# Kernel optimization log

Measured on AMD Instinct MI355X. Metric: run time of the kernel, lower is better.

The kernel has to match this reference:

```python
import jax, jax.numpy as jnp
import numpy as np

SIG = [1, 1, 1, 1, -1]  # Cl(4,1)
NVEC = 5
GA = 1 << NVEC  # 32


def _build_gp_table():
    # Cayley table for the geometric product on blades indexed by bitmask.
    G = np.zeros((GA, GA, GA), np.float32)
    for a in range(GA):
        for b in range(GA):
            s = 0
            t = a >> 1
            while t:
                s += bin(t & b).count('1')
                t >>= 1
            sign = -1.0 if (s & 1) else 1.0
            common = a & b
            for i in range(NVEC):
                if (common >> i) & 1:
                    sign *= SIG[i]
            G[a, b, a ^ b] = sign
    return G

GP_TABLE = jnp.asarray(_build_gp_table())


def geometric_product(x, y):
    return jnp.einsum('...i,...j,ijk->...k', x, y, GP_TABLE)


def manifold_norm(x):
    # normalize each multivector onto the unit sphere in R^32
    return x / (jnp.linalg.norm(x, axis=-1, keepdims=True) + 1e-6)


def versor_linear(x, W, b):
    # channel mixing shared across multivector components: x [..., in, ga]
    return jnp.einsum('...ig,oi->...og', x, W) + b


def layer_norm2d(x, w, b):
    # LayerNorm over last two dims [D, ga] jointly
    mu = jnp.mean(x, axis=(-2, -1), keepdims=True)
    var = jnp.var(x, axis=(-2, -1), keepdims=True)
    return (x - mu) / jnp.sqrt(var + 1e-5) * w + b


def attention(x, Wq, bq, Wk, bk, Wv, bv, Wo, bo, n_heads):
    B, S, D, G = x.shape
    dh = D // n_heads
    q = versor_linear(x, Wq, bq).reshape(B, S, n_heads, dh, G)
    k = versor_linear(x, Wk, bk).reshape(B, S, n_heads, dh, G)
    v = versor_linear(x, Wv, bv).reshape(B, S, n_heads, dh, G)
    scale = 1.0 / np.sqrt(dh * G).astype(np.float32)
    scores = jnp.einsum('bshdg,bthdg->bhst', q, k) * scale
    probs = jax.nn.softmax(scores, axis=-1)
    o = jnp.einsum('bhst,bthdg->bshdg', probs, v).reshape(B, S, D, G)
    return versor_linear(o, Wo, bo)


N_HEADS = 8


def forward(x, Wq, bq, Wk, bk, Wv, bv, Wo, bo, ln1_w, ln1_b, ln2_w, ln2_b,
            gamma1, gamma2, W1, b1, W2, b2, Wr, br, Wc, bc):
    L = Wq.shape[0]
    for l in range(L):
        h = attention(layer_norm2d(x, ln1_w[l], ln1_b[l]),
                      Wq[l], bq[l], Wk[l], bk[l], Wv[l], bv[l], Wo[l], bo[l], N_HEADS)
        x = manifold_norm(x + gamma1[l] * h)
        m = versor_linear(layer_norm2d(x, ln2_w[l], ln2_b[l]), W1[l], b1[l])
        m = versor_linear(jnp.tanh(m), W2[l], b2[l])
        x = manifold_norm(x + gamma2[l] * m)
    # RecursiveRotorAccumulator: log(S)-step inclusive scan of rotors
    delta = versor_linear(x, Wr, br)
    rot = 0.5 * delta
    rot = rot.at[..., 0].add(1.0)
    rot = manifold_norm(rot)
    S = x.shape[1]
    step = 1
    while step < S:
        left = rot[:, :-step]
        right = rot[:, step:]
        comb = manifold_norm(geometric_product(right, left))
        rot = jnp.concatenate([rot[:, :step], comb], axis=1)
        step *= 2
    pooled = rot[:, -1]  # [B, D, ga]
    logits = pooled.reshape(pooled.shape[0], -1) @ Wc.T + bc
    return logits


def setup_inputs() -> dict:
    key = jax.random.key(0)
    B, S, D, G, L, NC = 8, 256, 64, GA, 4, 1000
    E = 4 * D  # expansion hidden
    ks = jax.random.split(key, 16)
    sd = 0.02
    inp = {
        'x': jax.random.normal(ks[0], (B, S, D, G), jnp.float32),
        'Wq': jax.random.normal(ks[1], (L, D, D), jnp.float32) * sd,
        'bq': jnp.zeros((L, D, G), jnp.float32),
        'Wk': jax.random.normal(ks[2], (L, D, D), jnp.float32) * sd,
        'bk': jnp.zeros((L, D, G), jnp.float32),
        'Wv': jax.random.normal(ks[3], (L, D, D), jnp.float32) * sd,
        'bv': jnp.zeros((L, D, G), jnp.float32),
        'Wo': jax.random.normal(ks[4], (L, D, D), jnp.float32) * sd,
        'bo': jnp.zeros((L, D, G), jnp.float32),
        'ln1_w': jnp.ones((L, D, G), jnp.float32),
        'ln1_b': jnp.zeros((L, D, G), jnp.float32),
        'ln2_w': jnp.ones((L, D, G), jnp.float32),
        'ln2_b': jnp.zeros((L, D, G), jnp.float32),
        'gamma1': 1e-5 * jnp.ones((L, D, G), jnp.float32),
        'gamma2': 1e-5 * jnp.ones((L, D, G), jnp.float32),
        'W1': jax.random.normal(ks[5], (L, E, D), jnp.float32) * sd,
        'b1': jnp.zeros((L, E, G), jnp.float32),
        'W2': jax.random.normal(ks[6], (L, D, E), jnp.float32) * sd,
        'b2': jnp.zeros((L, D, G), jnp.float32),
        'Wr': jax.random.normal(ks[7], (D, D), jnp.float32) * sd,
        'br': jnp.zeros((D, G), jnp.float32),
        'Wc': jax.random.normal(ks[8], (NC, D * G), jnp.float32) * sd,
        'bc': jnp.zeros((NC,), jnp.float32),
    }
    return inp


def reference(x, Wq, bq, Wk, bk, Wv, bv, Wo, bo, ln1_w, ln1_b, ln2_w, ln2_b,
              gamma1, gamma2, W1, b1, W2, b2, Wr, br, Wc, bc):
    return forward(x, Wq, bq, Wk, bk, Wv, bv, Wo, bo, ln1_w, ln1_b, ln2_w, ln2_b,
                   gamma1, gamma2, W1, b1, W2, b2, Wr, br, Wc, bc)
```

## Files before the change

### kernel.cpp

```cpp
#include <hip/hip_runtime.h>
#include <hip/hip_bf16.h>

constexpr int kB  = 8;
constexpr int kS  = 256;
constexpr int kD  = 64;
constexpr int kG  = 32;
constexpr int kE  = 256;
constexpr int kNH = 8;
constexpr int kHD = 256;
constexpr int kDG = kD * kG;
constexpr int kT  = kB * kS;
constexpr int kNC = 1000;

using bf16x8 = __attribute__((ext_vector_type(8))) short;
using f32x4  = __attribute__((ext_vector_type(4))) float;

__device__ __forceinline__ short f2bf(float f) {
    unsigned u = __float_as_uint(f);
    unsigned r = (u + 0x7FFFu + ((u >> 16) & 1u)) >> 16;
    return (short)r;
}

__device__ __forceinline__ float tanh_fast(float x) {
    float a = fabsf(x);
    float e = __expf(-2.f * a);
    float d = 1.f + e;
    float r = __builtin_amdgcn_rcpf(d);
    r = r * (2.f - d * r);
    float t = (1.f - e) * r;
    return copysignf(t, x);
}

__global__ __launch_bounds__(256) void cvtw_kernel(
    const float* __restrict__ Wq, const float* __restrict__ Wk,
    const float* __restrict__ Wv, const float* __restrict__ Wo,
    const float* __restrict__ W1, const float* __restrict__ W2,
    unsigned short* __restrict__ dst) {
    int idx = (blockIdx.x * 256 + threadIdx.x) * 4;
    const float* src; int off;
    if      (idx <  16384) { src = Wq; off = 0; }
    else if (idx <  32768) { src = Wk; off = 16384; }
    else if (idx <  49152) { src = Wv; off = 32768; }
    else if (idx <  65536) { src = Wo; off = 49152; }
    else if (idx < 131072) { src = W1; off = 65536; }
    else                   { src = W2; off = 131072; }
    const float4 v = *(const float4*)(src + (idx - off));
    *(short4*)&dst[idx] = make_short4(f2bf(v.x), f2bf(v.y), f2bf(v.z), f2bf(v.w));
}

__global__ __launch_bounds__(256) void ln_kernel(const float* __restrict__ Xin,
                                                 const float* __restrict__ w,
                                                 const float* __restrict__ b,
                                                 unsigned short* __restrict__ A) {
    int t = blockIdx.x, tid = threadIdx.x;
    const float* xp = Xin + (size_t)t * kDG;
    __shared__ float r1[256], r2[256];
    __shared__ short st[32 * 72];
    float v[8], s = 0.f, ss = 0.f;
#pragma unroll
    for (int j = 0; j < 8; j++) {
        float x = xp[tid + j * 256];
        v[j] = x; s += x; ss += x * x;
    }
    r1[tid] = s; r2[tid] = ss; __syncthreads();
    for (int o = 128; o > 0; o >>= 1) {
        if (tid < o) { r1[tid] += r1[tid + o]; r2[tid] += r2[tid + o]; }
        __syncthreads();
    }
    float mean = r1[0] * (1.f / kDG);
    float var  = r2[0] * (1.f / kDG) - mean * mean;
    float rstd = rsqrtf(var + 1e-5f);
#pragma unroll
    for (int j = 0; j < 8; j++) {
        int jj = tid + j * 256;
        float val = (v[j] - mean) * rstd * w[jj] + b[jj];
        st[(jj & 31) * 72 + (jj >> 5)] = f2bf(val);
    }
    __syncthreads();
    bf16x8 ov = *(const bf16x8*)&st[(tid >> 3) * 72 + (tid & 7) * 8];
    *(bf16x8*)&A[(size_t)t * kDG + tid * 8] = ov;
}

__device__ __forceinline__ void epi_res_mn_ln(
    const f32x4 (&acc)[4][2], const float* __restrict__ bias,
    const float* __restrict__ Xin, float* __restrict__ Xout,
    const float* __restrict__ gamma,
    const float* __restrict__ lnw, const float* __restrict__ lnb,
    unsigned short* __restrict__ Aout, int tok, int l16, int quad, bool do_ln) {
    const size_t tb = (size_t)tok * kDG;
    float xv[4][2][4];
    float s = 0.f, ss = 0.f;
#pragma unroll
    for (int mt = 0; mt < 4; ++mt)
#pragma unroll
        for (int r = 0; r < 4; ++r) {
            int o = mt * 16 + quad * 4 + r;
            float vv[2]; float sq = 0.f;
#pragma unroll
            for (int nt = 0; nt < 2; ++nt) {
                int g = nt * 16 + l16;
                float h = acc[mt][nt][r] + bias[o * kG + g];
                float v = Xin[tb + o * kG + g] + gamma[o * kG + g] * h;
                vv[nt] = v; sq = fmaf(v, v, sq);
            }
#pragma unroll
            for (int off = 1; off < 16; off <<= 1) sq += __shfl_xor(sq, off, 64);
            float rn = 1.f / (sqrtf(sq) + 1e-6f);
#pragma unroll
            for (int nt = 0; nt < 2; ++nt) {
                int g = nt * 16 + l16;
                float x = vv[nt] * rn;
                xv[mt][nt][r] = x;
                Xout[tb + o * kG + g] = x;
                s += x; ss = fmaf(x, x, ss);
            }
        }
    if (!do_ln) return;
#pragma unroll
    for (int off = 1; off < 64; off <<= 1) {
        s += __shfl_xor(s, off, 64); ss += __shfl_xor(ss, off, 64);
    }
    float mean = s * (1.f / kDG);
    float var  = ss * (1.f / kDG) - mean * mean;
    float rstd = rsqrtf(var + 1e-5f);
    unsigned short* aop = Aout + tb;
#pragma unroll
    for (int mt = 0; mt < 4; ++mt)
#pragma unroll
        for (int nt = 0; nt < 2; ++nt) {
            int g = nt * 16 + l16;
            int o0 = mt * 16 + quad * 4;
            short4 s4;
#pragma unroll
            for (int r = 0; r < 4; ++r) {
                int o = o0 + r;
                float lv = (xv[mt][nt][r] - mean) * rstd * lnw[o * kG + g] + lnb[o * kG + g];
                (&s4.x)[r] = f2bf(lv);
            }
            *(short4*)&aop[g * kD + o0] = s4;
        }
}

__global__ __launch_bounds__(256) void vlinT_kernel(const float* __restrict__ X,
                                                    const float* __restrict__ W,
                                                    const float* __restrict__ bias,
                                                    float* __restrict__ OutT) {
    __shared__ float sx[kDG];
    __shared__ float sw[kD * kD];
    int t = blockIdx.x, tid = threadIdx.x;
    const float* xp = X + (size_t)t * kDG;
    for (int j = tid; j < kDG; j += 256) sx[j] = xp[j];
    for (int j = tid; j < kD * kD; j += 256) sw[j] = W[j];
    __syncthreads();
    int g = tid & 31, ob = tid >> 5;
    int b = t >> 8, s = t & 255;
    float* op = OutT + ((size_t)b * kD * kS + s) * kG;
    for (int o = ob; o < kD; o += 8) {
        float acc = bias[o * kG + g];
        const float* wr = sw + o * kD;
#pragma unroll
        for (int i = 0; i < kD; i++) acc += wr[i] * sx[i * kG + g];
        op[(size_t)o * kS * kG + g] = acc;
    }
}

template<bool DO_LN>
__global__ __launch_bounds__(64) void mlp_fused_kernel(
    const unsigned short* __restrict__ A,
    const unsigned short* __restrict__ W1h,
    const float* __restrict__ b1,
    const unsigned short* __restrict__ W2h,
    const float* __restrict__ b2,
    float* __restrict__ X, const float* __restrict__ gamma,
    const float* __restrict__ lnw, const float* __restrict__ lnb,
    unsigned short* __restrict__ Aout) {
    __shared__ short sM[32 * 256];
    const int lane = threadIdx.x;
    const int l16 = lane & 15, quad = lane >> 4;
    const int tok = blockIdx.x;

    const unsigned short* xp = A + (size_t)tok * kDG;
    bf16x8 bfr[2][2];
#pragma unroll
    for (int c = 0; c < 2; ++c)
#pragma unroll
        for (int nt = 0; nt < 2; ++nt)
            bfr[c][nt] = *(const bf16x8*)&xp[(nt * 16 + l16) * kD + c * 32 + quad * 8];

    char* mwB = (char*)sM;

#pragma unroll
    for (int half = 0; half < 2; ++half) {
        f32x4 acc[8][2];
#pragma unroll
        for (int mt = 0; mt < 8; ++mt)
#pragma unroll
            for (int nt = 0; nt < 2; ++nt) acc[mt][nt] = (f32x4){0.f, 0.f, 0.f, 0.f};

#pragma unroll
        for (int mt = 0; mt < 8; ++mt)
#pragma unroll
            for (int c = 0; c < 2; ++c) {
                int e16 = half * 8 + mt;
                bf16x8 afr = *(const bf16x8*)&W1h[(e16 * 16 + l16) * kD + c * 32 + quad * 8];
#pragma unroll
                for (int nt = 0; nt < 2; ++nt)
                    acc[mt][nt] = __builtin_amdgcn_mfma_f32_16x16x32_bf16(afr, bfr[c][nt], acc[mt][nt], 0, 0, 0);
            }

#pragma unroll
        for (int mt = 0; mt < 8; ++mt)
#pragma unroll
            for (int nt = 0; nt < 2; ++nt) {
                int g = nt * 16 + l16;
                int e0 = (half * 8 + mt) * 16 + quad * 4;
                short4 s4;
#pragma unroll
                for (int r = 0; r < 4; ++r)
                    (&s4.x)[r] = f2bf(tanh_fast(acc[mt][nt][r] + b1[(e0 + r) * kG + g]));
                unsigned boff = (unsigned)g * 512u + (((unsigned)(e0 * 2)) ^ (((unsigned)g & 7u) << 4));
                *(short4*)(mwB + boff) = s4;
            }
    }

    f32x4 acc2[4][2];
#pragma unroll
    for (int mt = 0; mt < 4; ++mt)
#pragma unroll
        for (int nt = 0; nt < 2; ++nt) acc2[mt][nt] = (f32x4){0.f, 0.f, 0.f, 0.f};

#pragma unroll
    for (int c = 0; c < 8; ++c) {
        bf16x8 bq[2];
#pragma unroll
        for (int nt = 0; nt < 2; ++nt) {
            int g = nt * 16 + l16;
            unsigned boff = (unsigned)g * 512u + (((unsigned)(c * 64 + quad * 16)) ^ (((unsigned)g & 7u) << 4));
            bq[nt] = *(const bf16x8*)(mwB + boff);
        }
#pragma unroll
        for (int mt = 0; mt < 4; ++mt) {
            bf16x8 afr = *(const bf16x8*)&W2h[(mt * 16 + l16) * kE + c * 32 + quad * 8];
#pragma unroll
            for (int nt = 0; nt < 2; ++nt)
                acc2[mt][nt] = __builtin_amdgcn_mfma_f32_16x16x32_bf16(afr, bq[nt], acc2[mt][nt], 0, 0, 0);
        }
    }

    epi_res_mn_ln(acc2, b2, X, X, gamma, lnw, lnb, Aout, tok, l16, quad, DO_LN);
}

__global__ __launch_bounds__(256, 3) void gemmWo_fused_kernel(
    const unsigned short* __restrict__ X, const unsigned short* __restrict__ Wh,
    const float* __restrict__ bias,
    const float* __restrict__ Xin, const float* __restrict__ gamma,
    const float* __restrict__ lnw, const float* __restrict__ lnb,
    float* __restrict__ Xout, unsigned short* __restrict__ Aout) {
    constexpr int WS = 64 + 8;
    __shared__ short sW[64 * WS];

    const int tid = threadIdx.x, wave = tid >> 6, lane = tid & 63;
    const int l16 = lane & 15, quad = lane >> 4;
    const int tok = blockIdx.x * 4 + wave;

    for (int j = tid * 8; j < 64 * 64; j += 2048) {
        int o = j >> 6, i = j & 63;
        *(bf16x8*)&sW[o * WS + i] = *(const bf16x8*)(Wh + j);
    }

    const unsigned short* xp = X + (size_t)tok * kDG;
    bf16x8 bfr[2][2];
#pragma unroll
    for (int c = 0; c < 2; ++c)
#pragma unroll
        for (int nt = 0; nt < 2; ++nt)
            bfr[c][nt] = *(const bf16x8*)&xp[(nt * 16 + l16) * kD + c * 32 + quad * 8];
    __syncthreads();

    f32x4 acc[4][2];
#pragma unroll
    for (int mt = 0; mt < 4; ++mt)
#pragma unroll
        for (int nt = 0; nt < 2; ++nt) acc[mt][nt] = (f32x4){0.f, 0.f, 0.f, 0.f};

#pragma unroll
    for (int mt = 0; mt < 4; ++mt)
#pragma unroll
        for (int c = 0; c < 2; ++c) {
            bf16x8 afr = *(const bf16x8*)&sW[(mt * 16 + l16) * WS + c * 32 + quad * 8];
#pragma unroll
            for (int nt = 0; nt < 2; ++nt)
                acc[mt][nt] = __builtin_amdgcn_mfma_f32_16x16x32_bf16(afr, bfr[c][nt], acc[mt][nt], 0, 0, 0);
        }

    epi_res_mn_ln(acc, bias, Xin, Xout, gamma, lnw, lnb, Aout, tok, l16, quad, true);
}

__global__ __launch_bounds__(256, 3) void gemm_qkv_kernel(
    const unsigned short* __restrict__ X,
    const unsigned short* __restrict__ Wqh, const unsigned short* __restrict__ Wkh,
    const unsigned short* __restrict__ Wvh,
    const float* __restrict__ bq, const float* __restrict__ bk, const float* __restrict__ bv,
    unsigned short* __restrict__ Q, unsigned short* __restrict__ K, unsigned short* __restrict__ V) {
    constexpr int WS = 64 + 8;
    __shared__ short sW[3 * 64 * WS];

    const int tid = threadIdx.x, wave = tid >> 6, lane = tid & 63;
    const int l16 = lane & 15, quad = lane >> 4;
    const int tok = blockIdx.x * 4 + wave;

    const unsigned short* Wp[3] = {Wqh, Wkh, Wvh};
#pragma unroll
    for (int w = 0; w < 3; ++w)
        for (int j = tid * 8; j < 64 * 64; j += 2048) {
            int o = j >> 6, i = j & 63;
            *(bf16x8*)&sW[w * 64 * WS + o * WS + i] = *(const bf16x8*)(Wp[w] + j);
        }

    const unsigned short* xp = X + (size_t)tok * kDG;
    bf16x8 bfr[2][2];
#pragma unroll
    for (int c = 0; c < 2; ++c)
#pragma unroll
        for (int nt = 0; nt < 2; ++nt)
            bfr[c][nt] = *(const bf16x8*)&xp[(nt * 16 + l16) * kD + c * 32 + quad * 8];
    __syncthreads();

    f32x4 acc[3][4][2];
#pragma unroll
    for (int w = 0; w < 3; ++w)
#pragma unroll
        for (int mt = 0; mt < 4; ++mt)
#pragma unroll
            for (int nt = 0; nt < 2; ++nt) acc[w][mt][nt] = (f32x4){0.f, 0.f, 0.f, 0.f};

#pragma unroll
    for (int w = 0; w < 3; ++w)
#pragma unroll
        for (int mt = 0; mt < 4; ++mt)
#pragma unroll
            for (int c = 0; c < 2; ++c) {
                bf16x8 afr = *(const bf16x8*)&sW[w * 64 * WS + (mt * 16 + l16) * WS + c * 32 + quad * 8];
#pragma unroll
                for (int nt = 0; nt < 2; ++nt)
                    acc[w][mt][nt] = __builtin_amdgcn_mfma_f32_16x16x32_bf16(afr, bfr[c][nt], acc[w][mt][nt], 0, 0, 0);
            }

    unsigned short* Op[3] = {Q, K, V};
    const float* Bp[3] = {bq, bk, bv};
#pragma unroll
    for (int w = 0; w < 3; ++w) {
        unsigned short* op = Op[w] + (size_t)tok * kDG;
#pragma unroll
        for (int mt = 0; mt < 4; ++mt)
#pragma unroll
            for (int nt = 0; nt < 2; ++nt) {
                int g = nt * 16 + l16;
#pragma unroll
                for (int r = 0; r < 4; ++r) {
                    int o = mt * 16 + quad * 4 + r;
                    op[o * kG + g] = (unsigned short)f2bf(acc[w][mt][nt][r] + Bp[w][o * kG + g]);
                }
            }
    }
}

constexpr int QSTR = 264;
constexpr int VSTR = 40;

__global__ __launch_bounds__(256) void attn_mfma_kernel(const unsigned short* __restrict__ Q,
                                                        const unsigned short* __restrict__ K,
                                                        const unsigned short* __restrict__ V,
                                                        unsigned short* __restrict__ O) {
    __shared__ short sQ[64 * QSTR];
    __shared__ short sKV[2][256 * VSTR];

    const int qt = blockIdx.x, h = blockIdx.y, b = blockIdx.z;
    const int tid = threadIdx.x;
    const int wave = tid >> 6, lane = tid & 63;
    const int l16 = lane & 15, quad = lane >> 4;

    const size_t bh = (size_t)b * kS * kDG + (size_t)h * kHD;

#pragma unroll
    for (int it = 0; it < 8; ++it) {
        int j = it * 2048 + tid * 8;
        int row = j >> 8, col = j & 255;
        *(bf16x8*)&sQ[row * QSTR + col] =
            *(const bf16x8*)(Q + bh + (size_t)(qt * 64 + row) * kDG + col);
    }
#pragma unroll
    for (int it = 0; it < 4; ++it) {
        int j = it * 2048 + tid * 8;
        int row = j >> 8, col = j & 255;
        *(bf16x8*)&sKV[0][row * QSTR + col] =
            *(const bf16x8*)(K + bh + (size_t)row * kDG + col);
    }
    __syncthreads();

    bf16x8 afrag[8];
    {
        int row = wave * 16 + l16;
#pragma unroll
        for (int c = 0; c < 8; ++c)
            afrag[c] = *(const bf16x8*)&sQ[row * QSTR + c * 32 + quad * 8];
    }

    f32x4 acc[16];
#pragma unroll
    for (int i = 0; i < 16; ++i) acc[i] = (f32x4){0.f, 0.f, 0.f, 0.f};

    for (int kt = 0; kt < 8; ++kt) {
        bf16x8 kpre[4];
        if (kt < 7) {
#pragma unroll
            for (int it = 0; it < 4; ++it) {
                int j = it * 2048 + tid * 8;
                int row = j >> 8, col = j & 255;
                kpre[it] = *(const bf16x8*)(K + bh + (size_t)((kt + 1) * 32 + row) * kDG + col);
            }
        }
        const short* kb = sKV[kt & 1];
#pragma unroll
        for (int nt = 0; nt < 2; ++nt) {
            int key = nt * 16 + l16;
            f32x4 a = acc[kt * 2 + nt];
#pragma unroll
            for (int c = 0; c < 8; ++c) {
                bf16x8 bfrag = *(const bf16x8*)&kb[key * QSTR + c * 32 + quad * 8];
                a = __builtin_amdgcn_mfma_f32_16x16x32_bf16(afrag[c], bfrag, a, 0, 0, 0);
            }
            acc[kt * 2 + nt] = a;
        }
        if (kt < 7) {
            short* nb = sKV[(kt + 1) & 1];
#pragma unroll
            for (int it = 0; it < 4; ++it) {
                int j = it * 2048 + tid * 8;
                int row = j >> 8, col = j & 255;
                *(bf16x8*)&nb[row * QSTR + col] = kpre[it];
            }
            __syncthreads();
        }
    }

    float inv[4];
#pragma unroll
    for (int r = 0; r < 4; ++r) {
        float m = -1e30f;
#pragma unroll
        for (int t = 0; t < 16; ++t) m = fmaxf(m, acc[t][r]);
#pragma unroll
        for (int off = 1; off < 16; off <<= 1) m = fmaxf(m, __shfl_xor(m, off, 16));
        float s = 0.f;
#pragma unroll
        for (int t = 0; t < 16; ++t) {
            float p = __expf((acc[t][r] - m) * 0.0625f);
            acc[t][r] = p; s += p;
        }
#pragma unroll
        for (int off = 1; off < 16; off <<= 1) s += __shfl_xor(s, off, 16);
        inv[r] = 1.f / s;
    }

#pragma unroll
    for (int t = 0; t < 16; ++t)
#pragma unroll
        for (int r = 0; r < 4; ++r)
            sQ[(wave * 16 + quad * 4 + r) * QSTR + t * 16 + l16] = f2bf(acc[t][r]);

    {
        int kb = tid >> 5;
#pragma unroll
        for (int it = 0; it < 2; ++it) {
            int db = (tid & 31) + it * 32;
            short4 vr[4];
#pragma unroll
            for (int r = 0; r < 4; ++r)
                vr[r] = *(const short4*)(V + bh + (size_t)(kb * 4 + r) * kDG + db * 4);
#pragma unroll
            for (int i = 0; i < 4; ++i) {
                short4 p = make_short4((&vr[0].x)[i], (&vr[1].x)[i],
                                       (&vr[2].x)[i], (&vr[3].x)[i]);
                *(short4*)&sKV[0][(db * 4 + i) * VSTR + kb * 4] = p;
            }
        }
    }
    __syncthreads();

    f32x4 oacc[16];
#pragma unroll
    for (int i = 0; i < 16; ++i) oacc[i] = (f32x4){0.f, 0.f, 0.f, 0.f};

    for (int vt = 0; vt < 8; ++vt) {
        short4 vpre[8];
        if (vt < 7) {
            int kb = tid >> 5;
#pragma unroll
            for (int it = 0; it < 2; ++it) {
                int db = (tid & 31) + it * 32;
#pragma unroll
                for (int r = 0; r < 4; ++r)
                    vpre[it * 4 + r] = *(const short4*)(V + bh + (size_t)((vt + 1) * 32 + kb * 4 + r) * kDG + db * 4);
            }
        }
        const short* vb = sKV[vt & 1];
        bf16x8 pfrag = *(const bf16x8*)&sQ[(wave * 16 + l16) * QSTR + vt * 32 + quad * 8];
#pragma unroll
        for (int dt = 0; dt < 16; ++dt) {
            bf16x8 vfrag = *(const bf16x8*)&vb[(dt * 16 + l16) * VSTR + quad * 8];
            oacc[dt] = __builtin_amdgcn_mfma_f32_16x16x32_bf16(pfrag, vfrag, oacc[dt], 0, 0, 0);
        }
        if (vt < 7) {
            short* nb = sKV[(vt + 1) & 1];
            int kb = tid >> 5;
#pragma unroll
            for (int it = 0; it < 2; ++it) {
                int db = (tid & 31) + it * 32;
#pragma unroll
                for (int i = 0; i < 4; ++i) {
                    short4 p = make_short4((&vpre[it * 4 + 0].x)[i], (&vpre[it * 4 + 1].x)[i],
                                           (&vpre[it * 4 + 2].x)[i], (&vpre[it * 4 + 3].x)[i]);
                    *(short4*)&nb[(db * 4 + i) * VSTR + kb * 4] = p;
                }
            }
            __syncthreads();
        }
    }

    {
        const size_t ob = (size_t)(b * kS + qt * 64 + wave * 16 + quad * 4) * kDG + h * 8;
#pragma unroll
        for (int gg = 0; gg < 2; ++gg) {
            int g = gg * 16 + l16;
#pragma unroll
            for (int r = 0; r < 4; ++r) {
                bf16x8 pk;
#pragma unroll
                for (int k = 0; k < 8; ++k)
                    pk[k] = f2bf(oacc[k * 2 + gg][r] * inv[r]);
                *(bf16x8*)&O[ob + (size_t)r * kDG + g * kD] = pk;
            }
        }
    }
}

constexpr int pc_ce(unsigned v) { int c = 0; while (v) { c += v & 1; v >>= 1; } return c; }
constexpr unsigned gp_mask_ce(int a) {
    unsigned m = 0;
    for (int c = 0; c < 32; ++c) {
        int b = a ^ c;
        int s = (a & b) >> 4;
        for (int t = a >> 1; t; t >>= 1) s += pc_ce(t & b);
        if (s & 1) m |= (1u << c);
    }
    return m;
}

template<int A>
__device__ __forceinline__ void gp_term(const float* x, const float* y, float* acc) {
    constexpr unsigned m = gp_mask_ce(A);
    const float xa = x[A], nxa = -xa;
#pragma unroll
    for (int c = 0; c < 32; ++c)
        acc[c] = fmaf(((m >> c) & 1u) ? nxa : xa, y[A ^ c], acc[c]);
}

__device__ __forceinline__ void gp_mn_t(const float* x, const float* y, float* out) {
    float acc[32];
#pragma unroll
    for (int c = 0; c < 32; ++c) acc[c] = 0.f;
    gp_term<0>(x, y, acc);  gp_term<1>(x, y, acc);  gp_term<2>(x, y, acc);  gp_term<3>(x, y, acc);
    gp_term<4>(x, y, acc);  gp_term<5>(x, y, acc);  gp_term<6>(x, y, acc);  gp_term<7>(x, y, acc);
    gp_term<8>(x, y, acc);  gp_term<9>(x, y, acc);  gp_term<10>(x, y, acc); gp_term<11>(x, y, acc);
    gp_term<12>(x, y, acc); gp_term<13>(x, y, acc); gp_term<14>(x, y, acc); gp_term<15>(x, y, acc);
    gp_term<16>(x, y, acc); gp_term<17>(x, y, acc); gp_term<18>(x, y, acc); gp_term<19>(x, y, acc);
    gp_term<20>(x, y, acc); gp_term<21>(x, y, acc); gp_term<22>(x, y, acc); gp_term<23>(x, y, acc);
    gp_term<24>(x, y, acc); gp_term<25>(x, y, acc); gp_term<26>(x, y, acc); gp_term<27>(x, y, acc);
    gp_term<28>(x, y, acc); gp_term<29>(x, y, acc); gp_term<30>(x, y, acc); gp_term<31>(x, y, acc);
    float ss = 0.f;
#pragma unroll
    for (int c = 0; c < 32; ++c) ss = fmaf(acc[c], acc[c], ss);
    float r = 1.f / (sqrtf(ss) + 1e-6f);
#pragma unroll
    for (int c = 0; c < 32; ++c) out[c] = acc[c] * r;
}

__device__ __forceinline__ void leaf_load(const float* base, float* v) {
#pragma unroll
    for (int i = 0; i < 8; ++i) {
        const float4 f = *(const float4*)(base + i * 4);
        v[i * 4 + 0] = 0.5f * f.x; v[i * 4 + 1] = 0.5f * f.y;
        v[i * 4 + 2] = 0.5f * f.z; v[i * 4 + 3] = 0.5f * f.w;
    }
    v[0] += 1.f;
    float ss = 0.f;
#pragma unroll
    for (int c = 0; c < 32; ++c) ss = fmaf(v[c], v[c], ss);
    float r = 1.f / (sqrtf(ss) + 1e-6f);
#pragma unroll
    for (int c = 0; c < 32; ++c) v[c] *= r;
}

__global__ __launch_bounds__(256) void scanreg_kernel(const float* __restrict__ DT,
                                                      float* __restrict__ pooled) {
    const int wave = threadIdx.x >> 6, lane = threadIdx.x & 63;
    const int seq = blockIdx.x * 4 + wave;
    const float* base = DT + ((size_t)seq * kS + lane * 4) * kG;

    float R[32], Y[32], P[32], Xa[32], Yb[32];

    leaf_load(base, R);
    for (int j = 1; j < 4; ++j) {
        leaf_load(base + j * kG, Y);
        gp_mn_t(Y, R, R);
    }

    for (int step = 1; step < 64; step <<= 1) {
        const bool up = lane & step;
#pragma unroll
        for (int c = 0; c < 32; ++c) P[c] = __shfl_xor(R[c], step, 64);
#pragma unroll
        for (int c = 0; c < 32; ++c) {
            Xa[c] = up ? R[c] : P[c];
            Yb[c] = up ? P[c] : R[c];
        }
        gp_mn_t(Xa, Yb, R);
    }

    if (lane == 0) {
        float* op = pooled + (size_t)seq * kG;
#pragma unroll
        for (int i = 0; i < 8; ++i)
            *(float4*)(op + i * 4) = make_float4(R[i * 4], R[i * 4 + 1], R[i * 4 + 2], R[i * 4 + 3]);
    }
}

__global__ __launch_bounds__(256) void cls2_kernel(const float* __restrict__ P,
                                                   const float* __restrict__ Wc,
                                                   const float* __restrict__ bc,
                                                   float* __restrict__ out) {
    __shared__ float sp[kB * kDG];
    const int tid = threadIdx.x, wave = tid >> 6, lane = tid & 63;
    for (int j = tid * 4; j < kB * kDG; j += 1024)
        *(float4*)&sp[j] = *(const float4*)(P + j);
    __syncthreads();

    const int c = blockIdx.x * 4 + wave;
    const float* w = Wc + (size_t)c * kDG;
    float acc[kB];
#pragma unroll
    for (int b = 0; b < kB; ++b) acc[b] = 0.f;
#pragma unroll
    for (int cc = 0; cc < 8; ++cc) {
        const float4 w4 = *(const float4*)(w + cc * 256 + lane * 4);
#pragma unroll
        for (int b = 0; b < kB; ++b) {
            const float4 p4 = *(const float4*)&sp[b * kDG + cc * 256 + lane * 4];
            acc[b] += w4.x * p4.x + w4.y * p4.y + w4.z * p4.z + w4.w * p4.w;
        }
    }
#pragma unroll
    for (int b = 0; b < kB; ++b)
#pragma unroll
        for (int off = 32; off > 0; off >>= 1) acc[b] += __shfl_xor(acc[b], off, 64);
    if (lane == 0) {
        float bias = bc[c];
#pragma unroll
        for (int b = 0; b < kB; ++b) out[b * kNC + c] = acc[b] + bias;
    }
}

extern "C" void kernel_launch(void* const* d_in, const int* in_sizes, int n_in,
                              void* d_out, int out_size, void* d_ws, size_t ws_size,
                              hipStream_t stream) {
    const float* x_in = (const float*)d_in[0];
    const float* Wq   = (const float*)d_in[1];
    const float* bq   = (const float*)d_in[2];
    const float* Wk   = (const float*)d_in[3];
    const float* bk   = (const float*)d_in[4];
    const float* Wv   = (const float*)d_in[5];
    const float* bv   = (const float*)d_in[6];
    const float* Wo   = (const float*)d_in[7];
    const float* bo   = (const float*)d_in[8];
    const float* ln1w = (const float*)d_in[9];
    const float* ln1b = (const float*)d_in[10];
    const float* ln2w = (const float*)d_in[11];
    const float* ln2b = (const float*)d_in[12];
    const float* gm1  = (const float*)d_in[13];
    const float* gm2  = (const float*)d_in[14];
    const float* W1   = (const float*)d_in[15];
    const float* b1   = (const float*)d_in[16];
    const float* W2   = (const float*)d_in[17];
    const float* b2   = (const float*)d_in[18];
    const float* Wr   = (const float*)d_in[19];
    const float* br   = (const float*)d_in[20];
    const float* Wc   = (const float*)d_in[21];
    const float* bc   = (const float*)d_in[22];

    const size_t NEL = (size_t)kT * kDG;
    float* F  = (float*)d_ws;
    float* X  = F;
    unsigned short* Abf = (unsigned short*)(F + NEL);
    unsigned short* Qh = (unsigned short*)(F + 2 * NEL);
    unsigned short* Kh = (unsigned short*)(F + 3 * NEL);
    unsigned short* Vh = (unsigned short*)(F + 4 * NEL);
    unsigned short* Wb = (unsigned short*)(F + 5 * NEL);
    float* pooled = F + 2 * NEL;
    float* DT = F + NEL;

    cvtw_kernel<<<192, 256, 0, stream>>>(Wq, Wk, Wv, Wo, W1, W2, Wb);
    unsigned short* Wqh = Wb;
    unsigned short* Wkh = Wb + 16384;
    unsigned short* Wvh = Wb + 32768;
    unsigned short* Woh = Wb + 49152;
    unsigned short* W1h = Wb + 65536;
    unsigned short* W2h = Wb + 131072;

    ln_kernel<<<kT, 256, 0, stream>>>(x_in, ln1w, ln1b, Abf);

    for (int l = 0; l < 4; l++) {
        gemm_qkv_kernel<<<kT / 4, 256, 0, stream>>>(Abf,
            Wqh + l * 4096, Wkh + l * 4096, Wvh + l * 4096,
            bq + l * kDG, bk + l * kDG, bv + l * kDG, Qh, Kh, Vh);
        attn_mfma_kernel<<<dim3(4, kNH, kB), 256, 0, stream>>>(Qh, Kh, Vh, Abf);
        gemmWo_fused_kernel<<<kT / 4, 256, 0, stream>>>(Abf, Woh + l * 4096, bo + l * kDG,
            l == 0 ? x_in : X, gm1 + l * kDG, ln2w + l * kDG, ln2b + l * kDG, X, Abf);
        if (l < 3)
            mlp_fused_kernel<true><<<kT, 64, 0, stream>>>(Abf,
                W1h + l * 16384, b1 + l * kE * kG, W2h + l * 16384, b2 + l * kDG,
                X, gm2 + l * kDG, ln1w + (l + 1) * kDG, ln1b + (l + 1) * kDG, Abf);
        else
            mlp_fused_kernel<false><<<kT, 64, 0, stream>>>(Abf,
                W1h + l * 16384, b1 + l * kE * kG, W2h + l * 16384, b2 + l * kDG,
                X, gm2 + l * kDG, nullptr, nullptr, nullptr);
    }

    vlinT_kernel<<<kT, 256, 0, stream>>>(X, Wr, br, DT);
    scanreg_kernel<<<kB * kD / 4, 256, 0, stream>>>(DT, pooled);
    cls2_kernel<<<kNC / 4, 256, 0, stream>>>(pooled, Wc, bc, (float*)d_out);
}
```

Baseline: 555.8 us.

## Store residual stream transposed and split MLP across two waves

```diff
diff --git a/kernel.cpp b/kernel.cpp
--- a/kernel.cpp
+++ b/kernel.cpp
@@ -48,19 +48,47 @@
     *(short4*)&dst[idx] = make_short4(f2bf(v.x), f2bf(v.y), f2bf(v.z), f2bf(v.w));
 }
 
+__global__ __launch_bounds__(256) void prep_tr_kernel(
+    const float* __restrict__ bq, const float* __restrict__ bk,
+    const float* __restrict__ bv, const float* __restrict__ bo,
+    const float* __restrict__ b2, const float* __restrict__ gm1,
+    const float* __restrict__ gm2, const float* __restrict__ ln2w,
+    const float* __restrict__ ln2b, const float* __restrict__ ln1w,
+    const float* __restrict__ ln1b, const float* __restrict__ b1,
+    float* __restrict__ dst) {
+    __shared__ float lt[32 * 257];
+    const int a = blockIdx.x >> 2, l = blockIdx.x & 3;
+    const float* srcs[12] = {bq, bk, bv, bo, b2, gm1, gm2, ln2w, ln2b, ln1w, ln1b, b1};
+    const int R  = (a == 11) ? 256 : 64;
+    const int sh = (a == 11) ? 8 : 6;
+    const float* src = srcs[a] + (size_t)l * R * 32;
+    float* out = dst + a * 8192 + l * R * 32;
+    const int tid = threadIdx.x;
+    for (int j = tid; j < R * 32; j += 256) lt[(j & 31) * (R + 1) + (j >> 5)] = src[j];
+    __syncthreads();
+    for (int k = tid; k < R * 32; k += 256) {
+        int g = k >> sh, r = k & (R - 1);
+        out[k] = lt[g * (R + 1) + r];
+    }
+}
+
 __global__ __launch_bounds__(256) void ln_kernel(const float* __restrict__ Xin,
                                                  const float* __restrict__ w,
                                                  const float* __restrict__ b,
-                                                 unsigned short* __restrict__ A) {
+                                                 unsigned short* __restrict__ A,
+                                                 float* __restrict__ XT) {
     int t = blockIdx.x, tid = threadIdx.x;
     const float* xp = Xin + (size_t)t * kDG;
     __shared__ float r1[256], r2[256];
     __shared__ short st[32 * 72];
+    __shared__ float xf[32 * 68];
     float v[8], s = 0.f, ss = 0.f;
 #pragma unroll
     for (int j = 0; j < 8; j++) {
         float x = xp[tid + j * 256];
         v[j] = x; s += x; ss += x * x;
+        int jj = tid + j * 256;
+        xf[(jj & 31) * 68 + (jj >> 5)] = x;
     }
     r1[tid] = s; r2[tid] = ss; __syncthreads();
     for (int o = 128; o > 0; o >>= 1) {
@@ -79,77 +107,86 @@
     __syncthreads();
     bf16x8 ov = *(const bf16x8*)&st[(tid >> 3) * 72 + (tid & 7) * 8];
     *(bf16x8*)&A[(size_t)t * kDG + tid * 8] = ov;
-}
-
-__device__ __forceinline__ void epi_res_mn_ln(
-    const f32x4 (&acc)[4][2], const float* __restrict__ bias,
-    const float* __restrict__ Xin, float* __restrict__ Xout,
-    const float* __restrict__ gamma,
-    const float* __restrict__ lnw, const float* __restrict__ lnb,
-    unsigned short* __restrict__ Aout, int tok, int l16, int quad, bool do_ln) {
-    const size_t tb = (size_t)tok * kDG;
-    float xv[4][2][4];
-    float s = 0.f, ss = 0.f;
-#pragma unroll
-    for (int mt = 0; mt < 4; ++mt)
-#pragma unroll
-        for (int r = 0; r < 4; ++r) {
-            int o = mt * 16 + quad * 4 + r;
-            float vv[2]; float sq = 0.f;
-#pragma unroll
-            for (int nt = 0; nt < 2; ++nt) {
-                int g = nt * 16 + l16;
-                float h = acc[mt][nt][r] + bias[o * kG + g];
-                float v = Xin[tb + o * kG + g] + gamma[o * kG + g] * h;
-                vv[nt] = v; sq = fmaf(v, v, sq);
-            }
-#pragma unroll
-            for (int off = 1; off < 16; off <<= 1) sq += __shfl_xor(sq, off, 64);
-            float rn = 1.f / (sqrtf(sq) + 1e-6f);
-#pragma unroll
-            for (int nt = 0; nt < 2; ++nt) {
-                int g = nt * 16 + l16;
-                float x = vv[nt] * rn;
-                xv[mt][nt][r] = x;
-                Xout[tb + o * kG + g] = x;
-                s += x; ss = fmaf(x, x, ss);
-            }
-        }
-    if (!do_ln) return;
-#pragma unroll
-    for (int off = 1; off < 64; off <<= 1) {
-        s += __shfl_xor(s, off, 64); ss += __shfl_xor(ss, off, 64);
-    }
-    float mean = s * (1.f / kDG);
-    float var  = ss * (1.f / kDG) - mean * mean;
-    float rstd = rsqrtf(var + 1e-5f);
-    unsigned short* aop = Aout + tb;
-#pragma unroll
-    for (int mt = 0; mt < 4; ++mt)
+    const int row = tid >> 3, col = (tid & 7) * 8;
+    float* xo = XT + (size_t)t * kDG + tid * 8;
+    *(float4*)(xo + 0) = *(const float4*)&xf[row * 68 + col + 0];
+    *(float4*)(xo + 4) = *(const float4*)&xf[row * 68 + col + 4];
+}
+
+template<int MT>
+__device__ __forceinline__ void epiT(
+    const f32x4 (&acc)[MT][2], const float* __restrict__ bT,
+    float* __restrict__ XTp, const float* __restrict__ gT,
+    int l16, int quad, int obase,
+    float& s, float& ss, float (&xv)[MT][2][4]) {
+    s = 0.f; ss = 0.f;
+#pragma unroll
+    for (int mt = 0; mt < MT; ++mt) {
+        int o0 = obase + mt * 16 + quad * 4;
+        float vv[2][4];
 #pragma unroll
         for (int nt = 0; nt < 2; ++nt) {
             int g = nt * 16 + l16;
-            int o0 = mt * 16 + quad * 4;
+            const float4 b4 = *(const float4*)&bT[g * kD + o0];
+            const float4 g4 = *(const float4*)&gT[g * kD + o0];
+            const float4 xi = *(const float4*)&XTp[g * kD + o0];
+#pragma unroll
+            for (int r = 0; r < 4; ++r)
+                vv[nt][r] = (&xi.x)[r] + (&g4.x)[r] * (acc[mt][nt][r] + (&b4.x)[r]);
+        }
+        float rn[4];
+#pragma unroll
+        for (int r = 0; r < 4; ++r) {
+            float sq = vv[0][r] * vv[0][r] + vv[1][r] * vv[1][r];
+#pragma unroll
+            for (int off = 1; off < 16; off <<= 1) sq += __shfl_xor(sq, off, 64);
+            rn[r] = 1.f / (sqrtf(sq) + 1e-6f);
+        }
+#pragma unroll
+        for (int nt = 0; nt < 2; ++nt) {
+            int g = nt * 16 + l16;
+            float4 xo;
+#pragma unroll
+            for (int r = 0; r < 4; ++r) {
+                float x = vv[nt][r] * rn[r];
+                (&xo.x)[r] = x; xv[mt][nt][r] = x;
+                s += x; ss = fmaf(x, x, ss);
+            }
+            *(float4*)&XTp[g * kD + o0] = xo;
+        }
+    }
+}
+
+template<int MT>
+__device__ __forceinline__ void lnT(
+    const float (&xv)[MT][2][4], const float* __restrict__ lwT,
+    const float* __restrict__ lbT, unsigned short* __restrict__ Aoutp,
+    int l16, int quad, int obase, float mean, float rstd) {
+#pragma unroll
+    for (int mt = 0; mt < MT; ++mt)
+#pragma unroll
+        for (int nt = 0; nt < 2; ++nt) {
+            int g = nt * 16 + l16;
+            int o0 = obase + mt * 16 + quad * 4;
+            const float4 w4 = *(const float4*)&lwT[g * kD + o0];
+            const float4 b4 = *(const float4*)&lbT[g * kD + o0];
             short4 s4;
 #pragma unroll
-            for (int r = 0; r < 4; ++r) {
-                int o = o0 + r;
-                float lv = (xv[mt][nt][r] - mean) * rstd * lnw[o * kG + g] + lnb[o * kG + g];
-                (&s4.x)[r] = f2bf(lv);
-            }
-            *(short4*)&aop[g * kD + o0] = s4;
-        }
-}
-
-__global__ __launch_bounds__(256) void vlinT_kernel(const float* __restrict__ X,
+            for (int r = 0; r < 4; ++r)
+                (&s4.x)[r] = f2bf((xv[mt][nt][r] - mean) * rstd * (&w4.x)[r] + (&b4.x)[r]);
+            *(short4*)&Aoutp[g * kD + o0] = s4;
+        }
+}
+
+__global__ __launch_bounds__(256) void vlinT_kernel(const float* __restrict__ XT,
                                                     const float* __restrict__ W,
                                                     const float* __restrict__ bias,
                                                     float* __restrict__ OutT) {
-    __shared__ float sx[kDG];
+    __shared__ float sx[32 * 65];
     __shared__ float sw[kD * kD];
     int t = blockIdx.x, tid = threadIdx.x;
-    const float* xp = X + (size_t)t * kDG;
-    for (int j = tid; j < kDG; j += 256) sx[j] = xp[j];
+    const float* xp = XT + (size_t)t * kDG;
+    for (int j = tid; j < kDG; j += 256) sx[(j >> 6) * 65 + (j & 63)] = xp[j];
     for (int j = tid; j < kD * kD; j += 256) sw[j] = W[j];
     __syncthreads();
     int g = tid & 31, ob = tid >> 5;
@@ -159,23 +196,26 @@
         float acc = bias[o * kG + g];
         const float* wr = sw + o * kD;
 #pragma unroll
-        for (int i = 0; i < kD; i++) acc += wr[i] * sx[i * kG + g];
+        for (int i = 0; i < kD; i++) acc += wr[i] * sx[g * 65 + i];
         op[(size_t)o * kS * kG + g] = acc;
     }
 }
 
 template<bool DO_LN>
-__global__ __launch_bounds__(64) void mlp_fused_kernel(
+__global__ __launch_bounds__(128, 4) void mlp_fused_kernel(
     const unsigned short* __restrict__ A,
     const unsigned short* __restrict__ W1h,
-    const float* __restrict__ b1,
+    const float* __restrict__ b1T,
     const unsigned short* __restrict__ W2h,
-    const float* __restrict__ b2,
-    float* __restrict__ X, const float* __restrict__ gamma,
-    const float* __restrict__ lnw, const float* __restrict__ lnb,
+    const float* __restrict__ b2T,
+    float* __restrict__ XT, const float* __restrict__ gmT,
+    const float* __restrict__ lwT, const float* __restrict__ lbT,
     unsigned short* __restrict__ Aout) {
-    __shared__ short sM[32 * 256];
-    const int lane = threadIdx.x;
+    constexpr int MS = 264;
+    __shared__ short sM[32 * MS];
+    __shared__ float sred[4];
+    const int tid = threadIdx.x;
+    const int w = tid >> 6, lane = tid & 63;
     const int l16 = lane & 15, quad = lane >> 4;
     const int tok = blockIdx.x;
 
@@ -187,45 +227,40 @@
         for (int nt = 0; nt < 2; ++nt)
             bfr[c][nt] = *(const bf16x8*)&xp[(nt * 16 + l16) * kD + c * 32 + quad * 8];
 
-    char* mwB = (char*)sM;
-
-#pragma unroll
-    for (int half = 0; half < 2; ++half) {
-        f32x4 acc[8][2];
-#pragma unroll
-        for (int mt = 0; mt < 8; ++mt)
-#pragma unroll
-            for (int nt = 0; nt < 2; ++nt) acc[mt][nt] = (f32x4){0.f, 0.f, 0.f, 0.f};
-
-#pragma unroll
-        for (int mt = 0; mt < 8; ++mt)
-#pragma unroll
-            for (int c = 0; c < 2; ++c) {
-                int e16 = half * 8 + mt;
-                bf16x8 afr = *(const bf16x8*)&W1h[(e16 * 16 + l16) * kD + c * 32 + quad * 8];
-#pragma unroll
-                for (int nt = 0; nt < 2; ++nt)
-                    acc[mt][nt] = __builtin_amdgcn_mfma_f32_16x16x32_bf16(afr, bfr[c][nt], acc[mt][nt], 0, 0, 0);
-            }
-
-#pragma unroll
-        for (int mt = 0; mt < 8; ++mt)
-#pragma unroll
-            for (int nt = 0; nt < 2; ++nt) {
-                int g = nt * 16 + l16;
-                int e0 = (half * 8 + mt) * 16 + quad * 4;
-                short4 s4;
-#pragma unroll
-                for (int r = 0; r < 4; ++r)
-                    (&s4.x)[r] = f2bf(tanh_fast(acc[mt][nt][r] + b1[(e0 + r) * kG + g]));
-                unsigned boff = (unsigned)g * 512u + (((unsigned)(e0 * 2)) ^ (((unsigned)g & 7u) << 4));
-                *(short4*)(mwB + boff) = s4;
-            }
-    }
-
-    f32x4 acc2[4][2];
-#pragma unroll
-    for (int mt = 0; mt < 4; ++mt)
+    f32x4 acc[8][2];
+#pragma unroll
+    for (int mt = 0; mt < 8; ++mt)
+#pragma unroll
+        for (int nt = 0; nt < 2; ++nt) acc[mt][nt] = (f32x4){0.f, 0.f, 0.f, 0.f};
+
+#pragma unroll
+    for (int mt = 0; mt < 8; ++mt)
+#pragma unroll
+        for (int c = 0; c < 2; ++c) {
+            bf16x8 afr = *(const bf16x8*)&W1h[((w * 8 + mt) * 16 + l16) * kD + c * 32 + quad * 8];
+#pragma unroll
+            for (int nt = 0; nt < 2; ++nt)
+                acc[mt][nt] = __builtin_amdgcn_mfma_f32_16x16x32_bf16(afr, bfr[c][nt], acc[mt][nt], 0, 0, 0);
+        }
+
+#pragma unroll
+    for (int mt = 0; mt < 8; ++mt)
+#pragma unroll
+        for (int nt = 0; nt < 2; ++nt) {
+            int g = nt * 16 + l16;
+            int e0 = (w * 8 + mt) * 16 + quad * 4;
+            const float4 b4 = *(const float4*)&b1T[g * kE + e0];
+            short4 s4;
+#pragma unroll
+            for (int r = 0; r < 4; ++r)
+                (&s4.x)[r] = f2bf(tanh_fast(acc[mt][nt][r] + (&b4.x)[r]));
+            *(short4*)&sM[g * MS + e0] = s4;
+        }
+    __syncthreads();
+
+    f32x4 acc2[2][2];
+#pragma unroll
+    for (int mt = 0; mt < 2; ++mt)
 #pragma unroll
         for (int nt = 0; nt < 2; ++nt) acc2[mt][nt] = (f32x4){0.f, 0.f, 0.f, 0.f};
 
@@ -233,29 +268,41 @@
     for (int c = 0; c < 8; ++c) {
         bf16x8 bq[2];
 #pragma unroll
-        for (int nt = 0; nt < 2; ++nt) {
-            int g = nt * 16 + l16;
-            unsigned boff = (unsigned)g * 512u + (((unsigned)(c * 64 + quad * 16)) ^ (((unsigned)g & 7u) << 4));
-            bq[nt] = *(const bf16x8*)(mwB + boff);
-        }
-#pragma unroll
-        for (int mt = 0; mt < 4; ++mt) {
-            bf16x8 afr = *(const bf16x8*)&W2h[(mt * 16 + l16) * kE + c * 32 + quad * 8];
+        for (int nt = 0; nt < 2; ++nt)
+            bq[nt] = *(const bf16x8*)&sM[(nt * 16 + l16) * MS + c * 32 + quad * 8];
+#pragma unroll
+        for (int mt = 0; mt < 2; ++mt) {
+            bf16x8 afr = *(const bf16x8*)&W2h[(w * 32 + mt * 16 + l16) * kE + c * 32 + quad * 8];
 #pragma unroll
             for (int nt = 0; nt < 2; ++nt)
                 acc2[mt][nt] = __builtin_amdgcn_mfma_f32_16x16x32_bf16(afr, bq[nt], acc2[mt][nt], 0, 0, 0);
         }
     }
 
-    epi_res_mn_ln(acc2, b2, X, X, gamma, lnw, lnb, Aout, tok, l16, quad, DO_LN);
+    const size_t tb = (size_t)tok * kDG;
+    float xv[2][2][4]; float s, ss;
+    epiT<2>(acc2, b2T, XT + tb, gmT, l16, quad, w * 32, s, ss, xv);
+    if (DO_LN) {
+#pragma unroll
+        for (int off = 1; off < 64; off <<= 1) {
+            s += __shfl_xor(s, off, 64); ss += __shfl_xor(ss, off, 64);
+        }
+        if (lane == 0) { sred[w] = s; sred[2 + w] = ss; }
+        __syncthreads();
+        float st = sred[0] + sred[1], sst = sred[2] + sred[3];
+        float mean = st * (1.f / kDG);
+        float var  = sst * (1.f / kDG) - mean * mean;
+        float rstd = rsqrtf(var + 1e-5f);
+        lnT<2>(xv, lwT, lbT, Aout + tb, l16, quad, w * 32, mean, rstd);
+    }
 }
 
 __global__ __launch_bounds__(256, 3) void gemmWo_fused_kernel(
     const unsigned short* __restrict__ X, const unsigned short* __restrict__ Wh,
-    const float* __restrict__ bias,
-    const float* __restrict__ Xin, const float* __restrict__ gamma,
-    const float* __restrict__ lnw, const float* __restrict__ lnb,
-    float* __restrict__ Xout, unsigned short* __restrict__ Aout) {
+    const float* __restrict__ bT,
+    float* __restrict__ XT, const float* __restrict__ gmT,
+    const float* __restrict__ lwT, const float* __restrict__ lbT,
+    unsigned short* __restrict__ Aout) {
     constexpr int WS = 64 + 8;
     __shared__ short sW[64 * WS];
 
@@ -293,14 +340,24 @@
                 acc[mt][nt] = __builtin_amdgcn_mfma_f32_16x16x32_bf16(afr, bfr[c][nt], acc[mt][nt], 0, 0, 0);
         }
 
-    epi_res_mn_ln(acc, bias, Xin, Xout, gamma, lnw, lnb, Aout, tok, l16, quad, true);
+    const size_t tb = (size_t)tok * kDG;
+    float xv[4][2][4]; float s, ss;
+    epiT<4>(acc, bT, XT + tb, gmT, l16, quad, 0, s, ss, xv);
+#pragma unroll
+    for (int off = 1; off < 64; off <<= 1) {
+        s += __shfl_xor(s, off, 64); ss += __shfl_xor(ss, off, 64);
+    }
+    float mean = s * (1.f / kDG);
+    float var  = ss * (1.f / kDG) - mean * mean;
+    float rstd = rsqrtf(var + 1e-5f);
+    lnT<4>(xv, lwT, lbT, Aout + tb, l16, quad, 0, mean, rstd);
 }
 
 __global__ __launch_bounds__(256, 3) void gemm_qkv_kernel(
     const unsigned short* __restrict__ X,
     const unsigned short* __restrict__ Wqh, const unsigned short* __restrict__ Wkh,
     const unsigned short* __restrict__ Wvh,
-    const float* __restrict__ bq, const float* __restrict__ bk, const float* __restrict__ bv,
+    const float* __restrict__ bqT, const float* __restrict__ bkT, const float* __restrict__ bvT,
     unsigned short* __restrict__ Q, unsigned short* __restrict__ K, unsigned short* __restrict__ V) {
     constexpr int WS = 64 + 8;
     __shared__ short sW[3 * 64 * WS];
@@ -347,7 +404,7 @@
             }
 
     unsigned short* Op[3] = {Q, K, V};
-    const float* Bp[3] = {bq, bk, bv};
+    const float* Bp[3] = {bqT, bkT, bvT};
 #pragma unroll
     for (int w = 0; w < 3; ++w) {
         unsigned short* op = Op[w] + (size_t)tok * kDG;
@@ -356,11 +413,11 @@
 #pragma unroll
             for (int nt = 0; nt < 2; ++nt) {
                 int g = nt * 16 + l16;
-#pragma unroll
-                for (int r = 0; r < 4; ++r) {
-                    int o = mt * 16 + quad * 4 + r;
-                    op[o * kG + g] = (unsigned short)f2bf(acc[w][mt][nt][r] + Bp[w][o * kG + g]);
-                }
+                int o0 = mt * 16 + quad * 4;
+                const float4 b4 = *(const float4*)&Bp[w][g * kD + o0];
+#pragma unroll
+                for (int r = 0; r < 4; ++r)
+                    op[(o0 + r) * kG + g] = (unsigned short)f2bf(acc[w][mt][nt][r] + (&b4.x)[r]);
             }
     }
 }
@@ -700,16 +757,19 @@
 
     const size_t NEL = (size_t)kT * kDG;
     float* F  = (float*)d_ws;
-    float* X  = F;
+    float* XT = F;
     unsigned short* Abf = (unsigned short*)(F + NEL);
     unsigned short* Qh = (unsigned short*)(F + 2 * NEL);
     unsigned short* Kh = (unsigned short*)(F + 3 * NEL);
     unsigned short* Vh = (unsigned short*)(F + 4 * NEL);
     unsigned short* Wb = (unsigned short*)(F + 5 * NEL);
+    float* PT = F + 3 * NEL + NEL / 2;
     float* pooled = F + 2 * NEL;
     float* DT = F + NEL;
 
     cvtw_kernel<<<192, 256, 0, stream>>>(Wq, Wk, Wv, Wo, W1, W2, Wb);
+    prep_tr_kernel<<<48, 256, 0, stream>>>(bq, bk, bv, bo, b2, gm1, gm2,
+                                           ln2w, ln2b, ln1w, ln1b, b1, PT);
     unsigned short* Wqh = Wb;
     unsigned short* Wkh = Wb + 16384;
     unsigned short* Wvh = Wb + 32768;
@@ -717,26 +777,39 @@
     unsigned short* W1h = Wb + 65536;
     unsigned short* W2h = Wb + 131072;
 
-    ln_kernel<<<kT, 256, 0, stream>>>(x_in, ln1w, ln1b, Abf);
+    auto bqT   = [&](int l) { return PT + 0     + l * 2048; };
+    auto bkT   = [&](int l) { return PT + 8192  + l * 2048; };
+    auto bvT   = [&](int l) { return PT + 16384 + l * 2048; };
+    auto boT   = [&](int l) { return PT + 24576 + l * 2048; };
+    auto b2T   = [&](int l) { return PT + 32768 + l * 2048; };
+    auto gm1T  = [&](int l) { return PT + 40960 + l * 2048; };
+    auto gm2T  = [&](int l) { return PT + 49152 + l * 2048; };
+    auto ln2wT = [&](int l) { return PT + 57344 + l * 2048; };
+    auto ln2bT = [&](int l) { return PT + 65536 + l * 2048; };
+    auto ln1wT = [&](int l) { return PT + 73728 + l * 2048; };
+    auto ln1bT = [&](int l) { return PT + 81920 + l * 2048; };
+    auto b1T   = [&](int l) { return PT + 90112 + l * 8192; };
+
+    ln_kernel<<<kT, 256, 0, stream>>>(x_in, ln1w, ln1b, Abf, XT);
 
     for (int l = 0; l < 4; l++) {
         gemm_qkv_kernel<<<kT / 4, 256, 0, stream>>>(Abf,
             Wqh + l * 4096, Wkh + l * 4096, Wvh + l * 4096,
-            bq + l * kDG, bk + l * kDG, bv + l * kDG, Qh, Kh, Vh);
+            bqT(l), bkT(l), bvT(l), Qh, Kh, Vh);
         attn_mfma_kernel<<<dim3(4, kNH, kB), 256, 0, stream>>>(Qh, Kh, Vh, Abf);
-        gemmWo_fused_kernel<<<kT / 4, 256, 0, stream>>>(Abf, Woh + l * 4096, bo + l * kDG,
-            l == 0 ? x_in : X, gm1 + l * kDG, ln2w + l * kDG, ln2b + l * kDG, X, Abf);
+        gemmWo_fused_kernel<<<kT / 4, 256, 0, stream>>>(Abf, Woh + l * 4096, boT(l),
+            XT, gm1T(l), ln2wT(l), ln2bT(l), Abf);
         if (l < 3)
-            mlp_fused_kernel<true><<<kT, 64, 0, stream>>>(Abf,
-                W1h + l * 16384, b1 + l * kE * kG, W2h + l * 16384, b2 + l * kDG,
-                X, gm2 + l * kDG, ln1w + (l + 1) * kDG, ln1b + (l + 1) * kDG, Abf);
+            mlp_fused_kernel<true><<<kT, 128, 0, stream>>>(Abf,
+                W1h + l * 16384, b1T(l), W2h + l * 16384, b2T(l),
+                XT, gm2T(l), ln1wT(l + 1), ln1bT(l + 1), Abf);
         else
-            mlp_fused_kernel<false><<<kT, 64, 0, stream>>>(Abf,
-                W1h + l * 16384, b1 + l * kE * kG, W2h + l * 16384, b2 + l * kDG,
-                X, gm2 + l * kDG, nullptr, nullptr, nullptr);
-    }
-
-    vlinT_kernel<<<kT, 256, 0, stream>>>(X, Wr, br, DT);
+            mlp_fused_kernel<false><<<kT, 128, 0, stream>>>(Abf,
+                W1h + l * 16384, b1T(l), W2h + l * 16384, b2T(l),
+                XT, gm2T(l), nullptr, nullptr, nullptr);
+    }
+
+    vlinT_kernel<<<kT, 256, 0, stream>>>(XT, Wr, br, DT);
     scanreg_kernel<<<kB * kD / 4, 256, 0, stream>>>(DT, pooled);
     cls2_kernel<<<kNC / 4, 256, 0, stream>>>(pooled, Wc, bc, (float*)d_out);
 }
```

Result: no change. 552.8 us (-0.5%).
